# Optimization experiments

Hardware: AMD Instinct MI355X
Metric: run time of the kernel (lower is better)

## Reference

```python
import jax, jax.numpy as jnp
import numpy as np

B, T, D, H, L, V, CTX = 4, 2048, 256, 8, 12, 256, 2048
HD = D // H


def _ln(x, w, b, eps=1e-5):
    m = x.mean(-1, keepdims=True)
    v = ((x - m) ** 2).mean(-1, keepdims=True)
    return (x - m) * jax.lax.rsqrt(v + eps) * w + b


def setup_inputs() -> dict:
    key = jax.random.key(0)
    ks = jax.random.split(key, 16)
    s = 0.02
    inp = {
        "x": jax.random.randint(ks[0], (B, T), 0, V, dtype=jnp.int32),
        "tok_embed": jax.random.normal(ks[1], (V, D), jnp.float32) * s,
        "pos_embed": jax.random.normal(ks[2], (CTX, D), jnp.float32) * s,
        # stacked per-layer params (leading axis = layer)
        "ln1_w": jnp.ones((L, D), jnp.float32),
        "ln1_b": jnp.zeros((L, D), jnp.float32),
        "qkv_w": jax.random.normal(ks[3], (L, D, 3 * D), jnp.float32) * s,
        "qkv_b": jnp.zeros((L, 3 * D), jnp.float32),
        "out_w": jax.random.normal(ks[4], (L, D, D), jnp.float32) * s,
        "out_b": jnp.zeros((L, D), jnp.float32),
        "ln2_w": jnp.ones((L, D), jnp.float32),
        "ln2_b": jnp.zeros((L, D), jnp.float32),
        "fc1_w": jax.random.normal(ks[5], (L, D, 4 * D), jnp.float32) * s,
        "fc1_b": jnp.zeros((L, 4 * D), jnp.float32),
        "fc2_w": jax.random.normal(ks[6], (L, 4 * D, D), jnp.float32) * s,
        "fc2_b": jnp.zeros((L, D), jnp.float32),
        "lnf_w": jnp.ones((D,), jnp.float32),
        "lnf_b": jnp.zeros((D,), jnp.float32),
        "head_w": jax.random.normal(ks[7], (D, V), jnp.float32) * s,
        "head_b": jnp.zeros((V,), jnp.float32),
    }
    return inp


def _forward(x, tok_embed, pos_embed, ln1_w, ln1_b, qkv_w, qkv_b, out_w, out_b,
             ln2_w, ln2_b, fc1_w, fc1_b, fc2_w, fc2_b, lnf_w, lnf_b, head_w, head_b):
    Tcur = x.shape[1]
    h = tok_embed[x] + pos_embed[:Tcur][None, :, :]  # (B,T,D)
    causal = jnp.triu(jnp.ones((Tcur, Tcur), bool), k=1)  # True above diagonal
    scale = jnp.sqrt(jnp.asarray(HD, h.dtype))

    def step(h, p):
        (l1w, l1b, qw, qb, ow, ob, l2w, l2b, f1w, f1b, f2w, f2b) = p
        # attention
        z = _ln(h, l1w, l1b)
        qkv = z @ qw + qb  # (B,T,3D)
        qkv = qkv.reshape(h.shape[0], Tcur, 3, H, HD)
        q, k, v = qkv[:, :, 0], qkv[:, :, 1], qkv[:, :, 2]  # (B,T,H,HD)
        attn = jnp.einsum('bqhd,bkhd->bhqk', q, k) / scale
        attn = jnp.where(causal, -jnp.inf, attn)
        attn = jax.nn.softmax(attn, axis=-1)
        o = jnp.einsum('bhqk,bkhd->bqhd', attn, v).reshape(h.shape[0], Tcur, D)
        h = h + o @ ow + ob
        # MLP (torch nn.GELU default = exact erf gelu)
        z = _ln(h, l2w, l2b)
        z = jax.nn.gelu(z @ f1w + f1b, approximate=False)
        h = h + z @ f2w + f2b
        return h, None

    params = (ln1_w, ln1_b, qkv_w, qkv_b, out_w, out_b,
              ln2_w, ln2_b, fc1_w, fc1_b, fc2_w, fc2_b)
    h, _ = jax.lax.scan(step, h, params)
    h = _ln(h, lnf_w, lnf_b)
    return h @ head_w + head_b  # (B,T,V)


def reference(x, tok_embed, pos_embed, ln1_w, ln1_b, qkv_w, qkv_b, out_w, out_b,
              ln2_w, ln2_b, fc1_w, fc1_b, fc2_w, fc2_b, lnf_w, lnf_b, head_w, head_b):
    return _forward(x, tok_embed, pos_embed, ln1_w, ln1_b, qkv_w, qkv_b, out_w, out_b,
                    ln2_w, ln2_b, fc1_w, fc1_b, fc2_w, fc2_b, lnf_w, lnf_b, head_w, head_b)
```

## Files before the change

kernel.cpp:

```cpp
#include <hip/hip_runtime.h>
#include <cstdint>

#define TT 2048
#define DD 256
#define HH 8
#define LL 12

typedef __attribute__((ext_vector_type(8))) short s16x8;
typedef __attribute__((ext_vector_type(4))) float f32x4;

__device__ __forceinline__ unsigned short f2bf(float f) {
  union { float f; unsigned u; } v; v.f = f;
  return (unsigned short)((v.u + 0x7FFFu + ((v.u >> 16) & 1u)) >> 16);
}

__device__ __forceinline__ unsigned cvtpk(float lo, float hi) {
  unsigned r;
  asm("v_cvt_pk_bf16_f32 %0, %1, %2" : "=v"(r) : "v"(lo), "v"(hi));
  return r;
}

__device__ __forceinline__ float geluf(float x) {
  return 0.5f * x * (1.0f + erff(x * 0.70710678118654752f));
}

__device__ __forceinline__ float fexp2(float x) {
  float r;
  asm("v_exp_f32 %0, %1" : "=v"(r) : "v"(x));
  return r;
}

__device__ __forceinline__ void gload16(const void* g, void* l) {
  __builtin_amdgcn_global_load_lds((const __attribute__((address_space(1))) unsigned int*)g,
                                   (__attribute__((address_space(3))) unsigned int*)l, 16, 0, 0);
}

__global__ __launch_bounds__(256) void k_embed(const int* __restrict__ x,
                                               const float* __restrict__ tok,
                                               const float* __restrict__ pos,
                                               float* __restrict__ h) {
  int i = blockIdx.x * 256 + threadIdx.x;
  int row = i >> 6, c = i & 63;
  int t = x[row];
  f32x4 tv = ((const f32x4*)(tok + (size_t)t * DD))[c];
  f32x4 pv = ((const f32x4*)(pos + (size_t)(row & (TT - 1)) * DD))[c];
  ((f32x4*)(h + (size_t)row * DD))[c] = tv + pv;
}

__global__ __launch_bounds__(256) void k_ln(const float* __restrict__ h,
                                            const float* __restrict__ wgt,
                                            const float* __restrict__ bia,
                                            unsigned short* __restrict__ z) {
  int row = blockIdx.x * 4 + (threadIdx.x >> 6);
  int lane = threadIdx.x & 63;
  f32x4 v = ((const f32x4*)(h + (size_t)row * DD))[lane];
  float s = v[0] + v[1] + v[2] + v[3];
#pragma unroll
  for (int m = 32; m; m >>= 1) s += __shfl_xor(s, m);
  float mean = s * (1.0f / DD);
  f32x4 d = v - mean;
  float s2 = d[0] * d[0] + d[1] * d[1] + d[2] * d[2] + d[3] * d[3];
#pragma unroll
  for (int m = 32; m; m >>= 1) s2 += __shfl_xor(s2, m);
  float inv = rsqrtf(s2 * (1.0f / DD) + 1e-5f);
  f32x4 wv = ((const f32x4*)wgt)[lane];
  f32x4 bv = ((const f32x4*)bia)[lane];
  float o0 = d[0] * inv * wv[0] + bv[0], o1 = d[1] * inv * wv[1] + bv[1];
  float o2 = d[2] * inv * wv[2] + bv[2], o3 = d[3] * inv * wv[3] + bv[3];
  unsigned long long u64 = (unsigned long long)cvtpk(o0, o1) |
                           ((unsigned long long)cvtpk(o2, o3) << 32);
  *(unsigned long long*)(z + (size_t)row * DD + lane * 4) = u64;
}

__global__ __launch_bounds__(256) void k_cast_all(const float* __restrict__ qw, const float* __restrict__ ow,
                                                  const float* __restrict__ f1, const float* __restrict__ f2,
                                                  unsigned short* __restrict__ dst) {
  __shared__ float Tt[32][33];
  const int l = blockIdx.y;
  const int t = blockIdx.x;
  const float* src;
  unsigned short* d;
  int K, N, tk, tn;
  if (t < 192) {
    src = qw + (size_t)l * 196608; d = dst + (size_t)l * 786432;
    K = 256; N = 768; tk = t / 24; tn = t % 24;
  } else if (t < 256) {
    int t2 = t - 192;
    src = ow + (size_t)l * 65536; d = dst + (size_t)l * 786432 + 196608;
    K = 256; N = 256; tk = t2 >> 3; tn = t2 & 7;
  } else if (t < 512) {
    int t3 = t - 256;
    src = f1 + (size_t)l * 262144; d = dst + (size_t)l * 786432 + 262144;
    K = 256; N = 1024; tk = t3 >> 5; tn = t3 & 31;
  } else {
    int t4 = t - 512;
    src = f2 + (size_t)l * 262144; d = dst + (size_t)l * 786432 + 524288;
    K = 1024; N = 256; tk = t4 >> 3; tn = t4 & 7;
  }
  const int tx = threadIdx.x & 31, ty = threadIdx.x >> 5;
#pragma unroll
  for (int r = 0; r < 4; ++r) {
    int row = ty + r * 8;
    Tt[row][tx] = src[(size_t)(tk * 32 + row) * N + tn * 32 + tx];
  }
  __syncthreads();
#pragma unroll
  for (int r = 0; r < 4; ++r) {
    int row = ty + r * 8;
    d[(size_t)(tn * 32 + row) * K + tk * 32 + tx] = f2bf(Tt[tx][row]);
  }
}

__global__ __launch_bounds__(256) void k_cast_tr4(const float* __restrict__ qw, const float* __restrict__ ow,
                                                  const float* __restrict__ f1, const float* __restrict__ f2,
                                                  unsigned short* __restrict__ dq, unsigned short* __restrict__ dO,
                                                  unsigned short* __restrict__ d1, unsigned short* __restrict__ d2) {
  int t0 = blockIdx.x * 256 + threadIdx.x;
  int stride = gridDim.x * 256;
  for (int i = t0; i < 196608; i += stride) dq[i] = f2bf(qw[(i & 255) * 768 + (i >> 8)]);
  for (int i = t0; i < 65536; i += stride) dO[i] = f2bf(ow[(i & 255) * 256 + (i >> 8)]);
  for (int i = t0; i < 262144; i += stride) d1[i] = f2bf(f1[(i & 255) * 1024 + (i >> 8)]);
  for (int i = t0; i < 262144; i += stride) d2[i] = f2bf(f2[(i & 1023) * 256 + (i >> 10)]);
}

__global__ __launch_bounds__(256) void k_cast_tr256(const float* __restrict__ src, unsigned short* __restrict__ dst) {
  int i = blockIdx.x * 256 + threadIdx.x;
  dst[i] = f2bf(src[(i & 255) * 256 + (i >> 8)]);
}

template <int MODE, int MI>
__global__ __launch_bounds__(256, 3) void k_gemm(const unsigned short* __restrict__ A,
                                                 const unsigned short* __restrict__ BT,
                                                 const float* __restrict__ bias,
                                                 void* out, const float* resid,
                                                 int M, int N, int K) {
  __shared__ __align__(16) unsigned short As[2][MI * 32 * 64];
  __shared__ __align__(16) unsigned short Bs[2][128 * 64];
  const int tid = threadIdx.x;
  const int lane = tid & 63, wv = tid >> 6;
  const int wr = wv >> 1, wc = wv & 1;
  const int l15 = lane & 15, g = lane >> 4;
  const int BM = MI * 32;
  const int tm = blockIdx.y, tn = blockIdx.x;
  f32x4 acc[MI][4] = {};
  const int nk = K >> 6;
  const unsigned short* Ag0 = A + (size_t)tm * BM * K;
  const unsigned short* Bg0 = BT + (size_t)tn * 128 * K;

#pragma unroll
  for (int it = 0; it < MI; ++it) {
    int c = it * 256 + tid;
    gload16(Ag0 + (size_t)(c >> 3) * K + (c & 7) * 8, As[0] + c * 8);
  }
#pragma unroll
  for (int it = 0; it < 4; ++it) {
    int c = it * 256 + tid;
    gload16(Bg0 + (size_t)(c >> 3) * K + (c & 7) * 8, Bs[0] + c * 8);
  }
  __syncthreads();

  int buf = 0;
  for (int kt = 0; kt < nk; ++kt) {
    const bool have_next = (kt + 1 < nk);
    if (have_next) {
#pragma unroll
      for (int it = 0; it < MI; ++it) {
        int c = it * 256 + tid;
        gload16(Ag0 + (size_t)(c >> 3) * K + (kt + 1) * 64 + (c & 7) * 8, As[buf ^ 1] + c * 8);
      }
#pragma unroll
      for (int it = 0; it < 4; ++it) {
        int c = it * 256 + tid;
        gload16(Bg0 + (size_t)(c >> 3) * K + (kt + 1) * 64 + (c & 7) * 8, Bs[buf ^ 1] + c * 8);
      }
    }
#pragma unroll
    for (int ks = 0; ks < 2; ++ks) {
      s16x8 af[MI], bf[4];
#pragma unroll
      for (int mi = 0; mi < MI; ++mi)
        af[mi] = *(const s16x8*)(As[buf] + (wr * MI * 16 + mi * 16 + l15) * 64 + ks * 32 + g * 8);
#pragma unroll
      for (int ni = 0; ni < 4; ++ni)
        bf[ni] = *(const s16x8*)(Bs[buf] + (wc * 64 + ni * 16 + l15) * 64 + ks * 32 + g * 8);
#pragma unroll
      for (int mi = 0; mi < MI; ++mi)
#pragma unroll
        for (int ni = 0; ni < 4; ++ni)
          acc[mi][ni] = __builtin_amdgcn_mfma_f32_16x16x32_bf16(af[mi], bf[ni], acc[mi][ni], 0, 0, 0);
    }
    if (have_next) {
      __syncthreads();
      buf ^= 1;
    }
  }
#pragma unroll
  for (int ni = 0; ni < 4; ++ni) {
    int col = tn * 128 + wc * 64 + ni * 16 + l15;
    float bv = bias[col];
#pragma unroll
    for (int mi = 0; mi < MI; ++mi) {
      int row0 = tm * BM + wr * MI * 16 + mi * 16 + g * 4;
#pragma unroll
      for (int r = 0; r < 4; ++r) {
        size_t idx = (size_t)(row0 + r) * N + col;
        float vvv = acc[mi][ni][r] + bv;
        if (MODE == 0) ((unsigned short*)out)[idx] = f2bf(vvv);
        else if (MODE == 1) ((unsigned short*)out)[idx] = f2bf(geluf(vvv));
        else ((float*)out)[idx] = vvv;
      }
    }
  }
}

template <int NK>
__global__ __launch_bounds__(256, 2) void k_gemm_ln(const unsigned short* __restrict__ A,
                                                    const unsigned short* __restrict__ BT,
                                                    const float* __restrict__ bias,
                                                    float* __restrict__ h,
                                                    const float* __restrict__ lnw,
                                                    const float* __restrict__ lnb,
                                                    unsigned short* __restrict__ z) {
  __shared__ __align__(16) unsigned short As[2][32 * 64];
  __shared__ __align__(16) unsigned short Bs[2][256 * 64];
  const int tid = threadIdx.x;
  const int lane = tid & 63, wc = tid >> 6;
  const int l15 = lane & 15, g = lane >> 4;
  const int tm = blockIdx.x;
  const int K = NK * 64;
  f32x4 acc[2][4] = {};
  const unsigned short* Ag0 = A + (size_t)tm * 32 * K;

  gload16(Ag0 + (size_t)(tid >> 3) * K + (tid & 7) * 8, As[0] + tid * 8);
#pragma unroll
  for (int it = 0; it < 8; ++it) {
    int c = it * 256 + tid;
    gload16(BT + (size_t)(c >> 3) * K + (c & 7) * 8, Bs[0] + c * 8);
  }
  __syncthreads();

  int buf = 0;
  for (int kt = 0; kt < NK; ++kt) {
    const bool have_next = (kt + 1 < NK);
    if (have_next) {
      gload16(Ag0 + (size_t)(tid >> 3) * K + (kt + 1) * 64 + (tid & 7) * 8, As[buf ^ 1] + tid * 8);
#pragma unroll
      for (int it = 0; it < 8; ++it) {
        int c = it * 256 + tid;
        gload16(BT + (size_t)(c >> 3) * K + (kt + 1) * 64 + (c & 7) * 8, Bs[buf ^ 1] + c * 8);
      }
    }
#pragma unroll
    for (int ks = 0; ks < 2; ++ks) {
      s16x8 af[2], bf[4];
#pragma unroll
      for (int mi = 0; mi < 2; ++mi)
        af[mi] = *(const s16x8*)(As[buf] + (mi * 16 + l15) * 64 + ks * 32 + g * 8);
#pragma unroll
      for (int ni = 0; ni < 4; ++ni)
        bf[ni] = *(const s16x8*)(Bs[buf] + (wc * 64 + ni * 16 + l15) * 64 + ks * 32 + g * 8);
#pragma unroll
      for (int mi = 0; mi < 2; ++mi)
#pragma unroll
        for (int ni = 0; ni < 4; ++ni)
          acc[mi][ni] = __builtin_amdgcn_mfma_f32_16x16x32_bf16(af[mi], bf[ni], acc[mi][ni], 0, 0, 0);
    }
    if (have_next) {
      __syncthreads();
      buf ^= 1;
    }
  }
  const int row0 = tm * 32;
  float hv[2][4][4];
  float psum[2][4] = {}, psq[2][4] = {};
#pragma unroll
  for (int mi = 0; mi < 2; ++mi)
#pragma unroll
    for (int ni = 0; ni < 4; ++ni) {
      int col = wc * 64 + ni * 16 + l15;
      float bv = bias[col];
#pragma unroll
      for (int r = 0; r < 4; ++r) {
        int row = row0 + mi * 16 + g * 4 + r;
        float v = acc[mi][ni][r] + bv + h[(size_t)row * DD + col];
        hv[mi][ni][r] = v;
        h[(size_t)row * DD + col] = v;
        psum[mi][r] += v;
        psq[mi][r] += v * v;
      }
    }
#pragma unroll
  for (int m = 1; m < 16; m <<= 1)
#pragma unroll
    for (int mi = 0; mi < 2; ++mi)
#pragma unroll
      for (int r = 0; r < 4; ++r) {
        psum[mi][r] += __shfl_xor(psum[mi][r], m);
        psq[mi][r] += __shfl_xor(psq[mi][r], m);
      }
  __syncthreads();
  float* red = (float*)&As[0][0];
  if (l15 == 0) {
#pragma unroll
    for (int mi = 0; mi < 2; ++mi)
#pragma unroll
      for (int r = 0; r < 4; ++r) {
        int rw = mi * 16 + g * 4 + r;
        red[wc * 32 + rw] = psum[mi][r];
        red[128 + wc * 32 + rw] = psq[mi][r];
      }
  }
  __syncthreads();
  float mean[2][4], inv[2][4];
#pragma unroll
  for (int mi = 0; mi < 2; ++mi)
#pragma unroll
    for (int r = 0; r < 4; ++r) {
      int rw = mi * 16 + g * 4 + r;
      float s = (red[rw] + red[32 + rw]) + (red[64 + rw] + red[96 + rw]);
      float q = (red[128 + rw] + red[160 + rw]) + (red[192 + rw] + red[224 + rw]);
      float mn = s * (1.0f / DD);
      mean[mi][r] = mn;
      inv[mi][r] = rsqrtf(q * (1.0f / DD) - mn * mn + 1e-5f);
    }
#pragma unroll
  for (int ni = 0; ni < 4; ++ni) {
    int col = wc * 64 + ni * 16 + l15;
    float wv = lnw[col], bv = lnb[col];
#pragma unroll
    for (int mi = 0; mi < 2; ++mi)
#pragma unroll
      for (int r = 0; r < 4; ++r) {
        int row = row0 + mi * 16 + g * 4 + r;
        z[(size_t)row * DD + col] = f2bf((hv[mi][ni][r] - mean[mi][r]) * inv[mi][r] * wv + bv);
      }
  }
}

__global__ __launch_bounds__(256, 2) void k_attn(const unsigned short* __restrict__ qkv,
                                                 unsigned short* __restrict__ o) {
  __shared__ __align__(16) unsigned short Ks[2][128 * 40];
  __shared__ __align__(16) unsigned short Vs[2][2 * 32 * 72];
  const int tid = threadIdx.x, lane = tid & 63, w = tid >> 6;
  const int l15 = lane & 15, g = lane >> 4;
  const int p = blockIdx.x;
  const int b = blockIdx.y >> 3, hh = blockIdx.y & 7;
  const size_t base = (size_t)b * TT * 768 + hh * 32;
  const float scl2 = 0.25503492f;
  const int qt0 = p, qt1 = 31 - p;
  const int nt0 = (qt0 >> 1) + 1;
  const int kr = tid >> 1, khf = tid & 1;
  const int vk = tid & 127, vdh = tid >> 7;
  const int vkh = vk >> 6, vklo = vk & 63;
  const int pko = w * 1280;
  const int pvo = ((w & 1) * 2 + (w >> 1)) * 1152;

  s16x8 qf0 = *(const s16x8*)(qkv + base + (size_t)(qt0 * 64 + w * 16 + l15) * 768 + g * 8);
  s16x8 qf1 = *(const s16x8*)(qkv + base + (size_t)(qt1 * 64 + w * 16 + l15) * 768 + g * 8);

  {
    const unsigned short* kp = qkv + base + (size_t)kr * 768 + 256 + khf * 16;
    s16x8 k0 = *(const s16x8*)kp;
    s16x8 k1 = *(const s16x8*)(kp + 8);
    const unsigned short* vp = qkv + base + (size_t)vk * 768 + 512 + vdh * 16;
    s16x8 v0 = *(const s16x8*)vp;
    s16x8 v1 = *(const s16x8*)(vp + 8);
    *(s16x8*)(Ks[0] + kr * 40 + khf * 16) = k0;
    *(s16x8*)(Ks[0] + kr * 40 + khf * 16 + 8) = k1;
    unsigned short* vb = Vs[0] + vkh * 2304;
#pragma unroll
    for (int e = 0; e < 8; ++e) {
      int d0 = vdh * 16 + e, d1 = vdh * 16 + 8 + e;
      vb[d0 * 72 + (vklo ^ (((d0 >> 3) & 3) << 4))] = (unsigned short)v0[e];
      vb[d1 * 72 + (vklo ^ (((d1 >> 3) & 3) << 4))] = (unsigned short)v1[e];
    }
  }
  __syncthreads();

  f32x4 accO[2] = {};
  float mM = -3.0e38f, ls = 0.f;

  for (int t = 0; t < 17; ++t) {
    const int buf = t & 1;
    const bool ph = (t >= nt0);
    const int qt = ph ? qt1 : qt0;
    const int j = ph ? t - nt0 : t;
    const bool have_next = (t + 1 < 17);
    unsigned short* p0 = Ks[buf ^ 1] + pko;
    unsigned short* p1 = Vs[buf ^ 1] + pvo;
    s16x8 k0n, k1n, v0n, v1n;
    if (have_next) {
      const int jn = (t + 1 >= nt0) ? t + 1 - nt0 : t + 1;
      const unsigned short* kp = qkv + base + (size_t)(jn * 128 + kr) * 768 + 256 + khf * 16;
      k0n = *(const s16x8*)kp;
      k1n = *(const s16x8*)(kp + 8);
      const unsigned short* vp = qkv + base + (size_t)(jn * 128 + vk) * 768 + 512 + vdh * 16;
      v0n = *(const s16x8*)vp;
      v1n = *(const s16x8*)(vp + 8);
    }
    const int rel = qt * 64 + w * 16 - j * 128;
    const bool full = (rel >= 127);
    int cbm = (rel + 15) >> 4; if (cbm > 7) cbm = 7;
    f32x4 st[8];
#pragma unroll
    for (int cb = 0; cb < 8; ++cb)
      if (cb <= cbm) {
        s16x8 kf = *(const s16x8*)(Ks[buf] + (cb * 16 + l15) * 40 + g * 8);
        f32x4 zz = {};
        st[cb] = __builtin_amdgcn_mfma_f32_16x16x32_bf16(kf, ph ? qf1 : qf0, zz, 0, 0, 0);
      }
    float rmax = -3.0e38f;
#pragma unroll
    for (int cb = 0; cb < 8; ++cb)
      if (cb <= cbm) {
        if (!full) {
#pragma unroll
          for (int r = 0; r < 4; ++r)
            if ((cb * 16 + g * 4 + r) > rel + l15) st[cb][r] = -3.0e38f;
        }
#pragma unroll
        for (int r = 0; r < 4; ++r) rmax = fmaxf(rmax, st[cb][r]);
      }
    rmax = fmaxf(rmax, __shfl_xor(rmax, 16));
    rmax = fmaxf(rmax, __shfl_xor(rmax, 32));
    const float rs = rmax * scl2;
    float al = 1.0f;
    if (!__all(rs <= mM + 11.5f)) {
      float nm = fmaxf(mM, rs);
      al = fexp2(mM - nm);
      mM = nm;
#pragma unroll
      for (int r = 0; r < 4; ++r) {
        float aw = __shfl(al, g * 4 + r);
        accO[0][r] *= aw;
        accO[1][r] *= aw;
      }
    }
    float rsum = 0.f;
#pragma unroll
    for (int cb = 0; cb < 8; ++cb)
      if (cb <= cbm) {
        float e0 = fexp2(fmaf(st[cb][0], scl2, -mM));
        float e1 = fexp2(fmaf(st[cb][1], scl2, -mM));
        float e2 = fexp2(fmaf(st[cb][2], scl2, -mM));
        float e3 = fexp2(fmaf(st[cb][3], scl2, -mM));
        rsum += (e0 + e1) + (e2 + e3);
        unsigned long long u = (unsigned long long)cvtpk(e0, e1) |
                               ((unsigned long long)cvtpk(e2, e3) << 32);
        *(unsigned long long*)(((cb >> 2) ? p1 : p0) + l15 * 72 + (cb & 3) * 16 + g * 4) = u;
      }
    if (cbm < 7 && !(cbm & 1)) {
      unsigned short* pz = ((cbm + 1) >> 2) ? p1 : p0;
      *(unsigned long long*)(pz + l15 * 72 + ((cbm + 1) & 3) * 16 + g * 4) = 0ULL;
    }
    rsum += __shfl_xor(rsum, 16);
    rsum += __shfl_xor(rsum, 32);
    ls = ls * al + rsum;
    asm volatile("s_waitcnt lgkmcnt(0)" ::: "memory");
    __builtin_amdgcn_sched_barrier(0);
    const int kcm = cbm >> 1;
#pragma unroll
    for (int kc = 0; kc < 4; ++kc)
      if (kc <= kcm) {
        s16x8 pa = *(const s16x8*)(((kc >> 1) ? p1 : p0) + l15 * 72 + (kc & 1) * 32 + g * 8);
        s16x8 bv0, bv1;
#pragma unroll
        for (int hb = 0; hb < 2; ++hb) {
          const int d = hb * 16 + l15;
          const int kxr = ((kc & 1) * 32 + g * 8) ^ (((d >> 3) & 3) << 4);
          if (hb == 0) bv0 = *(const s16x8*)(Vs[buf] + (kc >> 1) * 2304 + d * 72 + kxr);
          else bv1 = *(const s16x8*)(Vs[buf] + (kc >> 1) * 2304 + d * 72 + kxr);
        }
        accO[0] = __builtin_amdgcn_mfma_f32_16x16x32_bf16(pa, bv0, accO[0], 0, 0, 0);
        accO[1] = __builtin_amdgcn_mfma_f32_16x16x32_bf16(pa, bv1, accO[1], 0, 0, 0);
      }
    if (have_next) {
      *(s16x8*)(Ks[buf ^ 1] + kr * 40 + khf * 16) = k0n;
      *(s16x8*)(Ks[buf ^ 1] + kr * 40 + khf * 16 + 8) = k1n;
      unsigned short* vb = Vs[buf ^ 1] + vkh * 2304;
#pragma unroll
      for (int e = 0; e < 8; ++e) {
        int d0 = vdh * 16 + e, d1 = vdh * 16 + 8 + e;
        vb[d0 * 72 + (vklo ^ (((d0 >> 3) & 3) << 4))] = (unsigned short)v0n[e];
        vb[d1 * 72 + (vklo ^ (((d1 >> 3) & 3) << 4))] = (unsigned short)v1n[e];
      }
      __syncthreads();
    }
    if (t == nt0 - 1) {
      float invl = 1.0f / ls;
#pragma unroll
      for (int r = 0; r < 4; ++r) {
        float lv = __shfl(invl, g * 4 + r);
        int row = qt0 * 64 + w * 16 + g * 4 + r;
        o[(size_t)(b * TT + row) * DD + hh * 32 + l15] = f2bf(accO[0][r] * lv);
        o[(size_t)(b * TT + row) * DD + hh * 32 + 16 + l15] = f2bf(accO[1][r] * lv);
      }
      accO[0] = f32x4{};
      accO[1] = f32x4{};
      mM = -3.0e38f;
      ls = 0.f;
    }
  }
  {
    float invl = 1.0f / ls;
#pragma unroll
    for (int r = 0; r < 4; ++r) {
      float lv = __shfl(invl, g * 4 + r);
      int row = qt1 * 64 + w * 16 + g * 4 + r;
      o[(size_t)(b * TT + row) * DD + hh * 32 + l15] = f2bf(accO[0][r] * lv);
      o[(size_t)(b * TT + row) * DD + hh * 32 + 16 + l15] = f2bf(accO[1][r] * lv);
    }
  }
}

extern "C" void kernel_launch(void* const* d_in, const int* in_sizes, int n_in,
                              void* d_out, int out_size, void* d_ws, size_t ws_size,
                              hipStream_t stream) {
  const int* x = (const int*)d_in[0];
  const float* tok = (const float*)d_in[1];
  const float* pos = (const float*)d_in[2];
  const float* ln1w = (const float*)d_in[3];
  const float* ln1b = (const float*)d_in[4];
  const float* qkvw = (const float*)d_in[5];
  const float* qkvb = (const float*)d_in[6];
  const float* outw = (const float*)d_in[7];
  const float* outb = (const float*)d_in[8];
  const float* ln2w = (const float*)d_in[9];
  const float* ln2b = (const float*)d_in[10];
  const float* f1w = (const float*)d_in[11];
  const float* f1b = (const float*)d_in[12];
  const float* f2w = (const float*)d_in[13];
  const float* f2b = (const float*)d_in[14];
  const float* lnfw = (const float*)d_in[15];
  const float* lnfb = (const float*)d_in[16];
  const float* hw = (const float*)d_in[17];
  const float* hb = (const float*)d_in[18];

  char* ws = (char*)d_ws;
  float* h = (float*)(ws + 0);
  unsigned short* z = (unsigned short*)(ws + 8388608);
  unsigned short* qkvB = (unsigned short*)(ws + 12582912);
  unsigned short* ob = (unsigned short*)(ws + 25165824);
  unsigned short* a1 = (unsigned short*)(ws + 29360128);
  unsigned short* wAll = (unsigned short*)(ws + 46137344);
  const bool bigws = ws_size >= 65142784ULL;
  unsigned short* wh = (unsigned short*)(ws + (bigws ? 65011712 : 47710208));

  if (bigws)
    k_cast_all<<<dim3(768, 12), dim3(256), 0, stream>>>(qkvw, outw, f1w, f2w, wAll);
  k_cast_tr256<<<dim3(256), dim3(256), 0, stream>>>(hw, wh);
  k_embed<<<dim3(2048), dim3(256), 0, stream>>>(x, tok, pos, h);
  k_ln<<<dim3(2048), dim3(256), 0, stream>>>(h, ln1w, ln1b, z);

  for (int l = 0; l < LL; ++l) {
    unsigned short* wq = wAll + (size_t)(bigws ? l : 0) * 786432;
    unsigned short* wo = wq + 196608;
    unsigned short* w1 = wo + 65536;
    unsigned short* w2 = w1 + 262144;
    if (!bigws)
      k_cast_tr4<<<dim3(1024), dim3(256), 0, stream>>>(
          qkvw + (size_t)l * 196608, outw + (size_t)l * 65536,
          f1w + (size_t)l * 262144, f2w + (size_t)l * 262144, wq, wo, w1, w2);
    k_gemm<0, 2><<<dim3(6, 128), dim3(256), 0, stream>>>(z, wq, qkvb + l * 768, qkvB, nullptr, 8192, 768, 256);
    k_attn<<<dim3(16, 32), dim3(256), 0, stream>>>(qkvB, ob);
    k_gemm_ln<4><<<dim3(256), dim3(256), 0, stream>>>(ob, wo, outb + l * 256, h,
                                                      ln2w + l * 256, ln2b + l * 256, z);
    k_gemm<1, 2><<<dim3(8, 128), dim3(256), 0, stream>>>(z, w1, f1b + l * 1024, a1, nullptr, 8192, 1024, 256);
    const float* nw = (l == LL - 1) ? lnfw : ln1w + (l + 1) * 256;
    const float* nb = (l == LL - 1) ? lnfb : ln1b + (l + 1) * 256;
    k_gemm_ln<16><<<dim3(256), dim3(256), 0, stream>>>(a1, w2, f2b + l * 256, h, nw, nb, z);
  }

  k_gemm<3, 2><<<dim3(2, 128), dim3(256), 0, stream>>>(z, wh, hb, d_out, nullptr, 8192, 256, 256);
}
```

Before: 1.380 ms.

## Split paired query tiles into separate attention blocks with higher occupancy

The attention kernel previously had each block process two query tiles (p and 31-p), balanced so every block walked 17 key tiles. Now each block handles one query tile, the grid doubles to 1024 blocks, and the heaviest tiles are launched first (qt = 31 - blockIdx.x). Launch bounds rise to 4 blocks per CU so more waves can hide latency, at the cost of register pressure, possible spills and uneven per-block work.

```diff
diff --git a/kernel.cpp b/kernel.cpp
--- a/kernel.cpp
+++ b/kernel.cpp
@@ -337,26 +337,24 @@
   }
 }
 
-__global__ __launch_bounds__(256, 2) void k_attn(const unsigned short* __restrict__ qkv,
+__global__ __launch_bounds__(256, 4) void k_attn(const unsigned short* __restrict__ qkv,
                                                  unsigned short* __restrict__ o) {
   __shared__ __align__(16) unsigned short Ks[2][128 * 40];
   __shared__ __align__(16) unsigned short Vs[2][2 * 32 * 72];
   const int tid = threadIdx.x, lane = tid & 63, w = tid >> 6;
   const int l15 = lane & 15, g = lane >> 4;
-  const int p = blockIdx.x;
+  const int qt = 31 - blockIdx.x;
   const int b = blockIdx.y >> 3, hh = blockIdx.y & 7;
   const size_t base = (size_t)b * TT * 768 + hh * 32;
   const float scl2 = 0.25503492f;
-  const int qt0 = p, qt1 = 31 - p;
-  const int nt0 = (qt0 >> 1) + 1;
+  const int nt = (qt >> 1) + 1;
   const int kr = tid >> 1, khf = tid & 1;
   const int vk = tid & 127, vdh = tid >> 7;
   const int vkh = vk >> 6, vklo = vk & 63;
   const int pko = w * 1280;
   const int pvo = ((w & 1) * 2 + (w >> 1)) * 1152;
 
-  s16x8 qf0 = *(const s16x8*)(qkv + base + (size_t)(qt0 * 64 + w * 16 + l15) * 768 + g * 8);
-  s16x8 qf1 = *(const s16x8*)(qkv + base + (size_t)(qt1 * 64 + w * 16 + l15) * 768 + g * 8);
+  s16x8 qf = *(const s16x8*)(qkv + base + (size_t)(qt * 64 + w * 16 + l15) * 768 + g * 8);
 
   {
     const unsigned short* kp = qkv + base + (size_t)kr * 768 + 256 + khf * 16;
@@ -380,25 +378,21 @@
   f32x4 accO[2] = {};
   float mM = -3.0e38f, ls = 0.f;
 
-  for (int t = 0; t < 17; ++t) {
+  for (int t = 0; t < nt; ++t) {
     const int buf = t & 1;
-    const bool ph = (t >= nt0);
-    const int qt = ph ? qt1 : qt0;
-    const int j = ph ? t - nt0 : t;
-    const bool have_next = (t + 1 < 17);
+    const bool have_next = (t + 1 < nt);
     unsigned short* p0 = Ks[buf ^ 1] + pko;
     unsigned short* p1 = Vs[buf ^ 1] + pvo;
     s16x8 k0n, k1n, v0n, v1n;
     if (have_next) {
-      const int jn = (t + 1 >= nt0) ? t + 1 - nt0 : t + 1;
-      const unsigned short* kp = qkv + base + (size_t)(jn * 128 + kr) * 768 + 256 + khf * 16;
+      const unsigned short* kp = qkv + base + (size_t)((t + 1) * 128 + kr) * 768 + 256 + khf * 16;
       k0n = *(const s16x8*)kp;
       k1n = *(const s16x8*)(kp + 8);
-      const unsigned short* vp = qkv + base + (size_t)(jn * 128 + vk) * 768 + 512 + vdh * 16;
+      const unsigned short* vp = qkv + base + (size_t)((t + 1) * 128 + vk) * 768 + 512 + vdh * 16;
       v0n = *(const s16x8*)vp;
       v1n = *(const s16x8*)(vp + 8);
     }
-    const int rel = qt * 64 + w * 16 - j * 128;
+    const int rel = qt * 64 + w * 16 - t * 128;
     const bool full = (rel >= 127);
     int cbm = (rel + 15) >> 4; if (cbm > 7) cbm = 7;
     f32x4 st[8];
@@ -407,7 +401,7 @@
       if (cb <= cbm) {
         s16x8 kf = *(const s16x8*)(Ks[buf] + (cb * 16 + l15) * 40 + g * 8);
         f32x4 zz = {};
-        st[cb] = __builtin_amdgcn_mfma_f32_16x16x32_bf16(kf, ph ? qf1 : qf0, zz, 0, 0, 0);
+        st[cb] = __builtin_amdgcn_mfma_f32_16x16x32_bf16(kf, qf, zz, 0, 0, 0);
       }
     float rmax = -3.0e38f;
 #pragma unroll
@@ -486,27 +480,13 @@
       }
       __syncthreads();
     }
-    if (t == nt0 - 1) {
-      float invl = 1.0f / ls;
-#pragma unroll
-      for (int r = 0; r < 4; ++r) {
-        float lv = __shfl(invl, g * 4 + r);
-        int row = qt0 * 64 + w * 16 + g * 4 + r;
-        o[(size_t)(b * TT + row) * DD + hh * 32 + l15] = f2bf(accO[0][r] * lv);
-        o[(size_t)(b * TT + row) * DD + hh * 32 + 16 + l15] = f2bf(accO[1][r] * lv);
-      }
-      accO[0] = f32x4{};
-      accO[1] = f32x4{};
-      mM = -3.0e38f;
-      ls = 0.f;
-    }
   }
   {
     float invl = 1.0f / ls;
 #pragma unroll
     for (int r = 0; r < 4; ++r) {
       float lv = __shfl(invl, g * 4 + r);
-      int row = qt1 * 64 + w * 16 + g * 4 + r;
+      int row = qt * 64 + w * 16 + g * 4 + r;
       o[(size_t)(b * TT + row) * DD + hh * 32 + l15] = f2bf(accO[0][r] * lv);
       o[(size_t)(b * TT + row) * DD + hh * 32 + 16 + l15] = f2bf(accO[1][r] * lv);
     }
@@ -562,7 +542,7 @@
           qkvw + (size_t)l * 196608, outw + (size_t)l * 65536,
           f1w + (size_t)l * 262144, f2w + (size_t)l * 262144, wq, wo, w1, w2);
     k_gemm<0, 2><<<dim3(6, 128), dim3(256), 0, stream>>>(z, wq, qkvb + l * 768, qkvB, nullptr, 8192, 768, 256);
-    k_attn<<<dim3(16, 32), dim3(256), 0, stream>>>(qkvB, ob);
+    k_attn<<<dim3(32, 32), dim3(256), 0, stream>>>(qkvB, ob);
     k_gemm_ln<4><<<dim3(256), dim3(256), 0, stream>>>(ob, wo, outb + l * 256, h,
                                                       ln2w + l * 256, ln2b + l * 256, z);
     k_gemm<1, 2><<<dim3(8, 128), dim3(256), 0, stream>>>(z, w1, f1b + l * 1024, a1, nullptr, 8192, 1024, 256);
```

After: 1.471 ms. 6.6% more time.

## Split attention key tile across wave pairs with split-softmax merge

Applied to the files above, without the earlier changes.

The attention block grows from 4 to 8 waves. Each pair of waves splits the 128-key tile into two 64-key halves and keeps separate online-softmax state for each half. At each output point, the partial accumulators, max and sum are written to shared memory and merged by the first wave of each pair. The goal is more parallelism and latency hiding per block, since the grid has only 512 blocks. The cost is extra syncthreads, shared-memory scratch traffic for the merge, and higher register and occupancy pressure from launch_bounds(512,4).

```diff
diff --git a/kernel.cpp b/kernel.cpp
--- a/kernel.cpp
+++ b/kernel.cpp
@@ -337,11 +337,12 @@
   }
 }
 
-__global__ __launch_bounds__(256, 2) void k_attn(const unsigned short* __restrict__ qkv,
+__global__ __launch_bounds__(512, 4) void k_attn(const unsigned short* __restrict__ qkv,
                                                  unsigned short* __restrict__ o) {
   __shared__ __align__(16) unsigned short Ks[2][128 * 40];
   __shared__ __align__(16) unsigned short Vs[2][2 * 32 * 72];
-  const int tid = threadIdx.x, lane = tid & 63, w = tid >> 6;
+  const int tid = threadIdx.x, lane = tid & 63, wvi = tid >> 6;
+  const int w = wvi >> 1, kh = wvi & 1;
   const int l15 = lane & 15, g = lane >> 4;
   const int p = blockIdx.x;
   const int b = blockIdx.y >> 3, hh = blockIdx.y & 7;
@@ -349,30 +350,30 @@
   const float scl2 = 0.25503492f;
   const int qt0 = p, qt1 = 31 - p;
   const int nt0 = (qt0 >> 1) + 1;
-  const int kr = tid >> 1, khf = tid & 1;
-  const int vk = tid & 127, vdh = tid >> 7;
-  const int vkh = vk >> 6, vklo = vk & 63;
-  const int pko = w * 1280;
-  const int pvo = ((w & 1) * 2 + (w >> 1)) * 1152;
+  const int krow = (wvi & 3) * 32 + (lane >> 1);
+  const int khK = lane & 1;
+  const int iv = wvi & 3;
+  const int khv = iv >> 1, dh = iv & 1;
 
   s16x8 qf0 = *(const s16x8*)(qkv + base + (size_t)(qt0 * 64 + w * 16 + l15) * 768 + g * 8);
   s16x8 qf1 = *(const s16x8*)(qkv + base + (size_t)(qt1 * 64 + w * 16 + l15) * 768 + g * 8);
 
-  {
-    const unsigned short* kp = qkv + base + (size_t)kr * 768 + 256 + khf * 16;
+  if (wvi < 4) {
+    const unsigned short* kp = qkv + base + (size_t)krow * 768 + 256 + khK * 16;
     s16x8 k0 = *(const s16x8*)kp;
     s16x8 k1 = *(const s16x8*)(kp + 8);
-    const unsigned short* vp = qkv + base + (size_t)vk * 768 + 512 + vdh * 16;
+    *(s16x8*)(Ks[0] + krow * 40 + khK * 16) = k0;
+    *(s16x8*)(Ks[0] + krow * 40 + khK * 16 + 8) = k1;
+  } else {
+    const unsigned short* vp = qkv + base + (size_t)(khv * 64 + lane) * 768 + 512 + dh * 16;
     s16x8 v0 = *(const s16x8*)vp;
     s16x8 v1 = *(const s16x8*)(vp + 8);
-    *(s16x8*)(Ks[0] + kr * 40 + khf * 16) = k0;
-    *(s16x8*)(Ks[0] + kr * 40 + khf * 16 + 8) = k1;
-    unsigned short* vb = Vs[0] + vkh * 2304;
+    unsigned short* vb = Vs[0] + khv * 2304;
 #pragma unroll
     for (int e = 0; e < 8; ++e) {
-      int d0 = vdh * 16 + e, d1 = vdh * 16 + 8 + e;
-      vb[d0 * 72 + (vklo ^ (((d0 >> 3) & 3) << 4))] = (unsigned short)v0[e];
-      vb[d1 * 72 + (vklo ^ (((d1 >> 3) & 3) << 4))] = (unsigned short)v1[e];
+      int d0 = dh * 16 + e, d1 = dh * 16 + 8 + e;
+      vb[d0 * 72 + (lane ^ (((d0 >> 3) & 3) << 4))] = (unsigned short)v0[e];
+      vb[d1 * 72 + (lane ^ (((d1 >> 3) & 3) << 4))] = (unsigned short)v1[e];
     }
   }
   __syncthreads();
@@ -386,115 +387,142 @@
     const int qt = ph ? qt1 : qt0;
     const int j = ph ? t - nt0 : t;
     const bool have_next = (t + 1 < 17);
-    unsigned short* p0 = Ks[buf ^ 1] + pko;
-    unsigned short* p1 = Vs[buf ^ 1] + pvo;
+    unsigned short* ps = (wvi < 4) ? (Ks[buf ^ 1] + wvi * 1280)
+                                   : (Vs[buf ^ 1] + (wvi - 4) * 1152);
     s16x8 k0n, k1n, v0n, v1n;
     if (have_next) {
       const int jn = (t + 1 >= nt0) ? t + 1 - nt0 : t + 1;
-      const unsigned short* kp = qkv + base + (size_t)(jn * 128 + kr) * 768 + 256 + khf * 16;
-      k0n = *(const s16x8*)kp;
-      k1n = *(const s16x8*)(kp + 8);
-      const unsigned short* vp = qkv + base + (size_t)(jn * 128 + vk) * 768 + 512 + vdh * 16;
-      v0n = *(const s16x8*)vp;
-      v1n = *(const s16x8*)(vp + 8);
+      if (wvi < 4) {
+        const unsigned short* kp = qkv + base + (size_t)(jn * 128 + krow) * 768 + 256 + khK * 16;
+        k0n = *(const s16x8*)kp;
+        k1n = *(const s16x8*)(kp + 8);
+      } else {
+        const unsigned short* vp = qkv + base + (size_t)(jn * 128 + khv * 64 + lane) * 768 + 512 + dh * 16;
+        v0n = *(const s16x8*)vp;
+        v1n = *(const s16x8*)(vp + 8);
+      }
     }
     const int rel = qt * 64 + w * 16 - j * 128;
-    const bool full = (rel >= 127);
-    int cbm = (rel + 15) >> 4; if (cbm > 7) cbm = 7;
-    f32x4 st[8];
-#pragma unroll
-    for (int cb = 0; cb < 8; ++cb)
-      if (cb <= cbm) {
-        s16x8 kf = *(const s16x8*)(Ks[buf] + (cb * 16 + l15) * 40 + g * 8);
-        f32x4 zz = {};
-        st[cb] = __builtin_amdgcn_mfma_f32_16x16x32_bf16(kf, ph ? qf1 : qf0, zz, 0, 0, 0);
-      }
-    float rmax = -3.0e38f;
-#pragma unroll
-    for (int cb = 0; cb < 8; ++cb)
-      if (cb <= cbm) {
-        if (!full) {
-#pragma unroll
-          for (int r = 0; r < 4; ++r)
-            if ((cb * 16 + g * 4 + r) > rel + l15) st[cb][r] = -3.0e38f;
-        }
-#pragma unroll
-        for (int r = 0; r < 4; ++r) rmax = fmaxf(rmax, st[cb][r]);
-      }
-    rmax = fmaxf(rmax, __shfl_xor(rmax, 16));
-    rmax = fmaxf(rmax, __shfl_xor(rmax, 32));
-    const float rs = rmax * scl2;
-    float al = 1.0f;
-    if (!__all(rs <= mM + 11.5f)) {
-      float nm = fmaxf(mM, rs);
-      al = fexp2(mM - nm);
-      mM = nm;
-#pragma unroll
-      for (int r = 0; r < 4; ++r) {
-        float aw = __shfl(al, g * 4 + r);
-        accO[0][r] *= aw;
-        accO[1][r] *= aw;
-      }
-    }
-    float rsum = 0.f;
-#pragma unroll
-    for (int cb = 0; cb < 8; ++cb)
-      if (cb <= cbm) {
-        float e0 = fexp2(fmaf(st[cb][0], scl2, -mM));
-        float e1 = fexp2(fmaf(st[cb][1], scl2, -mM));
-        float e2 = fexp2(fmaf(st[cb][2], scl2, -mM));
-        float e3 = fexp2(fmaf(st[cb][3], scl2, -mM));
-        rsum += (e0 + e1) + (e2 + e3);
-        unsigned long long u = (unsigned long long)cvtpk(e0, e1) |
-                               ((unsigned long long)cvtpk(e2, e3) << 32);
-        *(unsigned long long*)(((cb >> 2) ? p1 : p0) + l15 * 72 + (cb & 3) * 16 + g * 4) = u;
-      }
-    if (cbm < 7 && !(cbm & 1)) {
-      unsigned short* pz = ((cbm + 1) >> 2) ? p1 : p0;
-      *(unsigned long long*)(pz + l15 * 72 + ((cbm + 1) & 3) * 16 + g * 4) = 0ULL;
-    }
-    rsum += __shfl_xor(rsum, 16);
-    rsum += __shfl_xor(rsum, 32);
-    ls = ls * al + rsum;
-    asm volatile("s_waitcnt lgkmcnt(0)" ::: "memory");
-    __builtin_amdgcn_sched_barrier(0);
-    const int kcm = cbm >> 1;
-#pragma unroll
-    for (int kc = 0; kc < 4; ++kc)
-      if (kc <= kcm) {
-        s16x8 pa = *(const s16x8*)(((kc >> 1) ? p1 : p0) + l15 * 72 + (kc & 1) * 32 + g * 8);
-        s16x8 bv0, bv1;
-#pragma unroll
-        for (int hb = 0; hb < 2; ++hb) {
-          const int d = hb * 16 + l15;
-          const int kxr = ((kc & 1) * 32 + g * 8) ^ (((d >> 3) & 3) << 4);
-          if (hb == 0) bv0 = *(const s16x8*)(Vs[buf] + (kc >> 1) * 2304 + d * 72 + kxr);
-          else bv1 = *(const s16x8*)(Vs[buf] + (kc >> 1) * 2304 + d * 72 + kxr);
-        }
-        accO[0] = __builtin_amdgcn_mfma_f32_16x16x32_bf16(pa, bv0, accO[0], 0, 0, 0);
-        accO[1] = __builtin_amdgcn_mfma_f32_16x16x32_bf16(pa, bv1, accO[1], 0, 0, 0);
-      }
+    int cbg = (rel + 15) >> 4; if (cbg > 7) cbg = 7;
+    const int cbm = (cbg - kh * 4 > 3) ? 3 : cbg - kh * 4;
+    if (cbm >= 0) {
+      const bool fullw = (rel >= kh * 64 + 63);
+      f32x4 st[4];
+#pragma unroll
+      for (int c = 0; c < 4; ++c)
+        if (c <= cbm) {
+          s16x8 kf = *(const s16x8*)(Ks[buf] + (kh * 64 + c * 16 + l15) * 40 + g * 8);
+          f32x4 zz = {};
+          st[c] = __builtin_amdgcn_mfma_f32_16x16x32_bf16(kf, ph ? qf1 : qf0, zz, 0, 0, 0);
+        }
+      float rmax = -3.0e38f;
+#pragma unroll
+      for (int c = 0; c < 4; ++c)
+        if (c <= cbm) {
+          if (!fullw) {
+#pragma unroll
+            for (int r = 0; r < 4; ++r)
+              if ((kh * 64 + c * 16 + g * 4 + r) > rel + l15) st[c][r] = -3.0e38f;
+          }
+#pragma unroll
+          for (int r = 0; r < 4; ++r) rmax = fmaxf(rmax, st[c][r]);
+        }
+      rmax = fmaxf(rmax, __shfl_xor(rmax, 16));
+      rmax = fmaxf(rmax, __shfl_xor(rmax, 32));
+      const float rs = rmax * scl2;
+      float al = 1.0f;
+      if (!__all(rs <= mM + 11.5f)) {
+        float nm = fmaxf(mM, rs);
+        al = fexp2(mM - nm);
+        mM = nm;
+#pragma unroll
+        for (int r = 0; r < 4; ++r) {
+          float aw = __shfl(al, g * 4 + r);
+          accO[0][r] *= aw;
+          accO[1][r] *= aw;
+        }
+      }
+      float rsum = 0.f;
+#pragma unroll
+      for (int c = 0; c < 4; ++c)
+        if (c <= cbm) {
+          float e0 = fexp2(fmaf(st[c][0], scl2, -mM));
+          float e1 = fexp2(fmaf(st[c][1], scl2, -mM));
+          float e2 = fexp2(fmaf(st[c][2], scl2, -mM));
+          float e3 = fexp2(fmaf(st[c][3], scl2, -mM));
+          rsum += (e0 + e1) + (e2 + e3);
+          unsigned long long u = (unsigned long long)cvtpk(e0, e1) |
+                                 ((unsigned long long)cvtpk(e2, e3) << 32);
+          *(unsigned long long*)(ps + l15 * 72 + c * 16 + g * 4) = u;
+        }
+      if (cbm < 3 && !(cbm & 1))
+        *(unsigned long long*)(ps + l15 * 72 + (cbm + 1) * 16 + g * 4) = 0ULL;
+      rsum += __shfl_xor(rsum, 16);
+      rsum += __shfl_xor(rsum, 32);
+      ls = ls * al + rsum;
+      asm volatile("s_waitcnt lgkmcnt(0)" ::: "memory");
+      __builtin_amdgcn_sched_barrier(0);
+      const int kcm = cbm >> 1;
+#pragma unroll
+      for (int kc = 0; kc < 2; ++kc)
+        if (kc <= kcm) {
+          s16x8 pa = *(const s16x8*)(ps + l15 * 72 + kc * 32 + g * 8);
+          s16x8 bv0, bv1;
+#pragma unroll
+          for (int hb = 0; hb < 2; ++hb) {
+            const int d = hb * 16 + l15;
+            const int kx = (kc * 32 + g * 8) ^ (((d >> 3) & 3) << 4);
+            if (hb == 0) bv0 = *(const s16x8*)(Vs[buf] + kh * 2304 + d * 72 + kx);
+            else bv1 = *(const s16x8*)(Vs[buf] + kh * 2304 + d * 72 + kx);
+          }
+          accO[0] = __builtin_amdgcn_mfma_f32_16x16x32_bf16(pa, bv0, accO[0], 0, 0, 0);
+          accO[1] = __builtin_amdgcn_mfma_f32_16x16x32_bf16(pa, bv1, accO[1], 0, 0, 0);
+        }
+    }
     if (have_next) {
-      *(s16x8*)(Ks[buf ^ 1] + kr * 40 + khf * 16) = k0n;
-      *(s16x8*)(Ks[buf ^ 1] + kr * 40 + khf * 16 + 8) = k1n;
-      unsigned short* vb = Vs[buf ^ 1] + vkh * 2304;
-#pragma unroll
-      for (int e = 0; e < 8; ++e) {
-        int d0 = vdh * 16 + e, d1 = vdh * 16 + 8 + e;
-        vb[d0 * 72 + (vklo ^ (((d0 >> 3) & 3) << 4))] = (unsigned short)v0n[e];
-        vb[d1 * 72 + (vklo ^ (((d1 >> 3) & 3) << 4))] = (unsigned short)v1n[e];
+      if (wvi < 4) {
+        *(s16x8*)(Ks[buf ^ 1] + krow * 40 + khK * 16) = k0n;
+        *(s16x8*)(Ks[buf ^ 1] + krow * 40 + khK * 16 + 8) = k1n;
+      } else {
+        unsigned short* vb = Vs[buf ^ 1] + khv * 2304;
+#pragma unroll
+        for (int e = 0; e < 8; ++e) {
+          int d0 = dh * 16 + e, d1 = dh * 16 + 8 + e;
+          vb[d0 * 72 + (lane ^ (((d0 >> 3) & 3) << 4))] = (unsigned short)v0n[e];
+          vb[d1 * 72 + (lane ^ (((d1 >> 3) & 3) << 4))] = (unsigned short)v1n[e];
+        }
       }
       __syncthreads();
     }
     if (t == nt0 - 1) {
-      float invl = 1.0f / ls;
-#pragma unroll
-      for (int r = 0; r < 4; ++r) {
-        float lv = __shfl(invl, g * 4 + r);
-        int row = qt0 * 64 + w * 16 + g * 4 + r;
-        o[(size_t)(b * TT + row) * DD + hh * 32 + l15] = f2bf(accO[0][r] * lv);
-        o[(size_t)(b * TT + row) * DD + hh * 32 + 16 + l15] = f2bf(accO[1][r] * lv);
-      }
+      float* sc = (float*)((wvi < 4) ? (Ks[buf] + wvi * 1280) : (Vs[buf] + (wvi - 4) * 1152));
+#pragma unroll
+      for (int hb = 0; hb < 2; ++hb)
+#pragma unroll
+        for (int r = 0; r < 4; ++r) sc[(g * 4 + r) * 32 + hb * 16 + l15] = accO[hb][r];
+      if (g == 0) { sc[512 + l15] = mM; sc[528 + l15] = ls; }
+      __syncthreads();
+      if (kh == 0) {
+        const int pw = wvi + 1;
+        float* pb = (float*)((pw < 4) ? (Ks[buf] + pw * 1280) : (Vs[buf] + (pw - 4) * 1152));
+#pragma unroll
+        for (int r = 0; r < 4; ++r) {
+          int q = g * 4 + r;
+          float mA = __shfl(mM, q), lA = __shfl(ls, q);
+          float mB = pb[512 + q], lB = pb[528 + q];
+          float M = fmaxf(mA, mB);
+          float eA = fexp2(mA - M), eB = fexp2(mB - M);
+          float inv = 1.0f / (eA * lA + eB * lB);
+          int row = qt0 * 64 + w * 16 + q;
+#pragma unroll
+          for (int hb = 0; hb < 2; ++hb) {
+            float ob = pb[q * 32 + hb * 16 + l15];
+            float val = (eA * accO[hb][r] + eB * ob) * inv;
+            o[(size_t)(b * TT + row) * DD + hh * 32 + hb * 16 + l15] = f2bf(val);
+          }
+        }
+      }
+      __syncthreads();
       accO[0] = f32x4{};
       accO[1] = f32x4{};
       mM = -3.0e38f;
@@ -502,13 +530,33 @@
     }
   }
   {
-    float invl = 1.0f / ls;
-#pragma unroll
-    for (int r = 0; r < 4; ++r) {
-      float lv = __shfl(invl, g * 4 + r);
-      int row = qt1 * 64 + w * 16 + g * 4 + r;
-      o[(size_t)(b * TT + row) * DD + hh * 32 + l15] = f2bf(accO[0][r] * lv);
-      o[(size_t)(b * TT + row) * DD + hh * 32 + 16 + l15] = f2bf(accO[1][r] * lv);
+    __syncthreads();
+    float* sc = (float*)((wvi < 4) ? (Ks[0] + wvi * 1280) : (Vs[0] + (wvi - 4) * 1152));
+#pragma unroll
+    for (int hb = 0; hb < 2; ++hb)
+#pragma unroll
+      for (int r = 0; r < 4; ++r) sc[(g * 4 + r) * 32 + hb * 16 + l15] = accO[hb][r];
+    if (g == 0) { sc[512 + l15] = mM; sc[528 + l15] = ls; }
+    __syncthreads();
+    if (kh == 0) {
+      const int pw = wvi + 1;
+      float* pb = (float*)((pw < 4) ? (Ks[0] + pw * 1280) : (Vs[0] + (pw - 4) * 1152));
+#pragma unroll
+      for (int r = 0; r < 4; ++r) {
+        int q = g * 4 + r;
+        float mA = __shfl(mM, q), lA = __shfl(ls, q);
+        float mB = pb[512 + q], lB = pb[528 + q];
+        float M = fmaxf(mA, mB);
+        float eA = fexp2(mA - M), eB = fexp2(mB - M);
+        float inv = 1.0f / (eA * lA + eB * lB);
+        int row = qt1 * 64 + w * 16 + q;
+#pragma unroll
+        for (int hb = 0; hb < 2; ++hb) {
+          float ob = pb[q * 32 + hb * 16 + l15];
+          float val = (eA * accO[hb][r] + eB * ob) * inv;
+          o[(size_t)(b * TT + row) * DD + hh * 32 + hb * 16 + l15] = f2bf(val);
+        }
+      }
     }
   }
 }
@@ -562,7 +610,7 @@
           qkvw + (size_t)l * 196608, outw + (size_t)l * 65536,
           f1w + (size_t)l * 262144, f2w + (size_t)l * 262144, wq, wo, w1, w2);
     k_gemm<0, 2><<<dim3(6, 128), dim3(256), 0, stream>>>(z, wq, qkvb + l * 768, qkvB, nullptr, 8192, 768, 256);
-    k_attn<<<dim3(16, 32), dim3(256), 0, stream>>>(qkvB, ob);
+    k_attn<<<dim3(16, 32), dim3(512), 0, stream>>>(qkvB, ob);
     k_gemm_ln<4><<<dim3(256), dim3(256), 0, stream>>>(ob, wo, outb + l * 256, h,
                                                       ln2w + l * 256, ln2b + l * 256, z);
     k_gemm<1, 2><<<dim3(8, 128), dim3(256), 0, stream>>>(z, w1, f1b + l * 1024, a1, nullptr, 8192, 1024, 256);
```

New measurement: 1.288 ms (median of 4 runs). 6.7% less time.
